# Kernel tuning notes

Hardware: AMD Instinct MI355X
Metric: run time of the kernel (lower is better)

The kernel has to match this reference:

```python
import jax, jax.numpy as jnp
import numpy as np

B, N, K, H, NI = 8, 4096, 32, 128, 384
SCALE = 30.0
EPS = 1e-5


def _ln(x, g, b):
    m = jnp.mean(x, axis=-1, keepdims=True)
    v = jnp.mean(jnp.square(x - m), axis=-1, keepdims=True)
    return (x - m) * jax.lax.rsqrt(v + EPS) * g + b


def setup_inputs() -> dict:
    key = jax.random.key(0)
    ks = jax.random.split(key, 20)
    w = lambda k, shape: jax.random.normal(k, shape, jnp.float32) * 0.02
    return {
        "h_V": jax.random.normal(ks[0], (B, N, H), jnp.float32),
        "h_E": jax.random.normal(ks[1], (B, N, K, NI), jnp.float32),
        "mask_V": (jax.random.uniform(ks[2], (B, N)) > 0.1).astype(jnp.float32),
        "mask_attend": (jax.random.uniform(ks[3], (B, N, K)) > 0.1).astype(jnp.float32),
        "W1_w": w(ks[4], (H, H + NI)), "W1_b": jnp.zeros((H,), jnp.float32),
        "W2_w": w(ks[5], (H, H)), "W2_b": jnp.zeros((H,), jnp.float32),
        "W3_w": w(ks[6], (H, H)), "W3_b": jnp.zeros((H,), jnp.float32),
        "ln1_g": jnp.ones((H,), jnp.float32), "ln1_b": jnp.zeros((H,), jnp.float32),
        "ln2_g": jnp.ones((H,), jnp.float32), "ln2_b": jnp.zeros((H,), jnp.float32),
        "Win_w": w(ks[7], (4 * H, H)), "Win_b": jnp.zeros((4 * H,), jnp.float32),
        "Wout_w": w(ks[8], (H, 4 * H)), "Wout_b": jnp.zeros((H,), jnp.float32),
    }


def reference(h_V, h_E, mask_V, mask_attend,
              W1_w, W1_b, W2_w, W2_b, W3_w, W3_b,
              ln1_g, ln1_b, ln2_g, ln2_b,
              Win_w, Win_b, Wout_w, Wout_b):
    gelu = lambda x: jax.nn.gelu(x, approximate=False)  # torch exact GELU
    # Split W1 across the broadcast (h_V) and per-edge (h_E) inputs instead of
    # materializing the [B,N,K,H+NI] concat: identical math, less memory.
    W1v, W1e = W1_w[:, :H], W1_w[:, H:]
    hv_part = jnp.einsum('bnh,oh->bno', h_V, W1v)              # [B,N,H]
    he_part = jnp.einsum('bnke,oe->bnko', h_E, W1e)            # [B,N,K,H]
    m = gelu(hv_part[:, :, None, :] + he_part + W1_b)
    m = gelu(jnp.einsum('bnkh,oh->bnko', m, W2_w) + W2_b)
    m = jnp.einsum('bnkh,oh->bnko', m, W3_w) + W3_b            # h_message
    m = mask_attend[..., None] * m
    dh = jnp.sum(m, axis=-2) / SCALE                           # [B,N,H]
    h = _ln(h_V + dh, ln1_g, ln1_b)
    ff = jnp.einsum('bnf,of->bno', gelu(jnp.einsum('bnh,fh->bnf', h, Win_w) + Win_b), Wout_w) + Wout_b
    h = _ln(h + ff, ln2_g, ln2_b)
    return mask_V[..., None] * h
```

## Files before the change

kernel.cpp:

```cpp
#include <hip/hip_runtime.h>

#define NODES 32768

typedef __attribute__((ext_vector_type(8))) short bf16x8;
typedef __attribute__((ext_vector_type(4))) float f32x4;

__device__ __forceinline__ unsigned short f2bf(float f) {
  __bf16 b = (__bf16)f;
  return __builtin_bit_cast(unsigned short, b);
}

__device__ __forceinline__ unsigned char f2fp8(float x) {
  int v = __builtin_amdgcn_cvt_pk_fp8_f32(x, x, 0, false);
  return (unsigned char)(v & 0xff);
}
__device__ __forceinline__ unsigned int pk4(f32x4 v) {
  int r = __builtin_amdgcn_cvt_pk_fp8_f32(v[0], v[1], 0, false);
  r = __builtin_amdgcn_cvt_pk_fp8_f32(v[2], v[3], r, true);
  return (unsigned int)r;
}

__device__ __forceinline__ float gelu_f(float x) {
  float e = __builtin_amdgcn_exp2f(-2.4558673f * x);
  return x * __builtin_amdgcn_rcpf(1.0f + e);
}

__device__ __forceinline__ f32x4 mfma16(bf16x8 a, bf16x8 b, f32x4 c) {
  return __builtin_amdgcn_mfma_f32_16x16x32_bf16(a, b, c, 0, 0, 0);
}
__device__ __forceinline__ f32x4 mfma8(long a, long b, f32x4 c) {
  return __builtin_amdgcn_mfma_f32_16x16x32_fp8_fp8(a, b, c, 0, 0, 0);
}

__global__ void DecLayer_54357106098674_kernel() {}

__global__ __launch_bounds__(256) void pack_kernel(
    const float* __restrict__ W, unsigned short* __restrict__ out,
    int ctiles, int ld, int koff) {
  int ct = blockIdx.x % ctiles;
  int ks = blockIdx.x / ctiles;
#pragma unroll
  for (int h = 0; h < 2; ++h) {
    int idx = threadIdx.x + h * 256;
    int j = idx & 7;
    int lane = idx >> 3;
    int o = ct * 16 + (lane & 15);
    int k = ks * 32 + ((lane >> 4) << 3) + j;
    out[((size_t)blockIdx.x * 64 + lane) * 8 + j] = f2bf(W[(size_t)o * ld + koff + k]);
  }
}

__global__ __launch_bounds__(256) void pack8_kernel(
    const float* __restrict__ W, unsigned char* __restrict__ out,
    int ctiles, int ld, int koff) {
  int ct = blockIdx.x % ctiles;
  int ks = blockIdx.x / ctiles;
#pragma unroll
  for (int h = 0; h < 2; ++h) {
    int idx = threadIdx.x + h * 256;
    int j = idx & 7;
    int lane = idx >> 3;
    int o = ct * 16 + (lane & 15);
    int k = ks * 32 + ((lane >> 4) << 3) + j;
    out[((size_t)blockIdx.x * 64 + lane) * 8 + j] = f2fp8(W[(size_t)o * ld + koff + k]);
  }
}

__global__ __launch_bounds__(256, 6) void edge_kernel(
    const float* __restrict__ hE, const float* __restrict__ hV,
    const float* __restrict__ maskA,
    const unsigned short* __restrict__ W1vp,
    const unsigned char* __restrict__ W1e8,
    const unsigned char* __restrict__ W2p8,
    const unsigned char* __restrict__ W3p8,
    const float* __restrict__ W1bias,
    const float* __restrict__ W2bias, const float* __restrict__ W3bias,
    const float* __restrict__ ln1g, const float* __restrict__ ln1b,
    float* __restrict__ hb) {
  __shared__ __align__(16) unsigned char A8[64 * 392];
  __shared__ __align__(16) unsigned short hvb[2][136];
  __shared__ float mkl[64];
  unsigned char* m1 = A8;
  unsigned char* m2 = A8 + 8704;
  float* red2 = (float*)(A8 + 17408);

  const int t = threadIdx.x;
  const int pair = ((blockIdx.x & 7) << 11) | (blockIdx.x >> 3);
  const int node0 = pair * 2;
  const float* vb0 = hV + (size_t)node0 * 128;
  const float* vb1 = vb0 + 128;

  {
    const int rr = t >> 3, cc = t & 7;
    const f32x4* src = (const f32x4*)(hE + (size_t)node0 * 12288) + rr * 96 + cc;
    unsigned char* dst0 = &A8[rr * 392 + cc * 4];
#pragma unroll
    for (int i = 0; i < 12; ++i) {
      f32x4 v = __builtin_nontemporal_load(src + i * 8);
      *(unsigned int*)(dst0 + i * 32) = pk4(v);
    }
    const f32x4* src1 = src + 32 * 96;
    unsigned char* dst1 = &A8[(rr + 32) * 392 + cc * 4];
#pragma unroll
    for (int i = 0; i < 12; ++i) {
      f32x4 v = __builtin_nontemporal_load(src1 + i * 8);
      *(unsigned int*)(dst1 + i * 32) = pk4(v);
    }
  }
  if (t < 64) {
    int nn = t >> 5, s = t & 31;
    f32x4 v = ((const f32x4*)(hV + (size_t)(node0 + nn) * 128))[s];
    ushort4 u;
    u.x = f2bf(v[0]); u.y = f2bf(v[1]); u.z = f2bf(v[2]); u.w = f2bf(v[3]);
    *(ushort4*)&hvb[nn][s * 4] = u;
  } else if (t < 128) {
    int q = t - 64;
    mkl[q] = maskA[(size_t)node0 * 32 + q];
  }
  __syncthreads();

  const int w = t >> 6, l = t & 63, lr = l & 15, lk = l >> 4;
  const int ct0 = w * 2, ct1 = w * 2 + 1;
  const int c0 = ct0 * 16 + lr, c1 = ct1 * 16 + lr;

  f32x4 g0[4], g1[4];
#pragma unroll
  for (int rt = 0; rt < 4; ++rt) {
    g0[rt] = (f32x4){0.f, 0.f, 0.f, 0.f};
    g1[rt] = (f32x4){0.f, 0.f, 0.f, 0.f};
  }
#pragma unroll
  for (int ks = 0; ks < 4; ++ks) {
    bf16x8 w0 = *(const bf16x8*)&W1vp[((size_t)(ks * 8 + ct0) * 64 + l) * 8];
    bf16x8 w1 = *(const bf16x8*)&W1vp[((size_t)(ks * 8 + ct1) * 64 + l) * 8];
#pragma unroll
    for (int rt = 0; rt < 4; ++rt) {
      bf16x8 a = *(const bf16x8*)&hvb[rt >> 1][ks * 32 + lk * 8];
      g0[rt] = mfma16(a, w0, g0[rt]);
      g1[rt] = mfma16(a, w1, g1[rt]);
    }
  }
#pragma unroll
  for (int ks = 0; ks < 12; ++ks) {
    long w0 = *(const long*)&W1e8[((size_t)(ks * 8 + ct0) * 64 + l) * 8];
    long w1 = *(const long*)&W1e8[((size_t)(ks * 8 + ct1) * 64 + l) * 8];
#pragma unroll
    for (int rt = 0; rt < 4; ++rt) {
      long a = *(const long*)&A8[(rt * 16 + lr) * 392 + ks * 32 + lk * 8];
      g0[rt] = mfma8(a, w0, g0[rt]);
      g1[rt] = mfma8(a, w1, g1[rt]);
    }
  }
  __syncthreads();

  {
    float bb0 = W1bias[c0], bb1 = W1bias[c1];
#pragma unroll
    for (int rt = 0; rt < 4; ++rt) {
#pragma unroll
      for (int r = 0; r < 4; ++r) {
        int row = rt * 16 + lk * 4 + r;
        m1[row * 136 + c0] = f2fp8(gelu_f(g0[rt][r] + bb0));
        m1[row * 136 + c1] = f2fp8(gelu_f(g1[rt][r] + bb1));
      }
    }
  }
  __syncthreads();

  f32x4 d0[4], d1[4];
#pragma unroll
  for (int rt = 0; rt < 4; ++rt) {
    d0[rt] = (f32x4){0.f, 0.f, 0.f, 0.f};
    d1[rt] = (f32x4){0.f, 0.f, 0.f, 0.f};
  }
#pragma unroll
  for (int ks = 0; ks < 4; ++ks) {
    long w0 = *(const long*)&W2p8[((size_t)(ks * 8 + ct0) * 64 + l) * 8];
    long w1 = *(const long*)&W2p8[((size_t)(ks * 8 + ct1) * 64 + l) * 8];
#pragma unroll
    for (int rt = 0; rt < 4; ++rt) {
      long a = *(const long*)&m1[(rt * 16 + lr) * 136 + ks * 32 + lk * 8];
      d0[rt] = mfma8(a, w0, d0[rt]);
      d1[rt] = mfma8(a, w1, d1[rt]);
    }
  }
  {
    float bb0 = W2bias[c0], bb1 = W2bias[c1];
#pragma unroll
    for (int rt = 0; rt < 4; ++rt) {
#pragma unroll
      for (int r = 0; r < 4; ++r) {
        int row = rt * 16 + lk * 4 + r;
        m2[row * 136 + c0] = f2fp8(gelu_f(d0[rt][r] + bb0));
        m2[row * 136 + c1] = f2fp8(gelu_f(d1[rt][r] + bb1));
      }
    }
  }
  __syncthreads();

  f32x4 e0[4], e1[4];
#pragma unroll
  for (int rt = 0; rt < 4; ++rt) {
    e0[rt] = (f32x4){0.f, 0.f, 0.f, 0.f};
    e1[rt] = (f32x4){0.f, 0.f, 0.f, 0.f};
  }
#pragma unroll
  for (int ks = 0; ks < 4; ++ks) {
    long w0 = *(const long*)&W3p8[((size_t)(ks * 8 + ct0) * 64 + l) * 8];
    long w1 = *(const long*)&W3p8[((size_t)(ks * 8 + ct1) * 64 + l) * 8];
#pragma unroll
    for (int rt = 0; rt < 4; ++rt) {
      long a = *(const long*)&m2[(rt * 16 + lr) * 136 + ks * 32 + lk * 8];
      e0[rt] = mfma8(a, w0, e0[rt]);
      e1[rt] = mfma8(a, w1, e1[rt]);
    }
  }

  {
    float b30 = W3bias[c0], b31 = W3bias[c1];
    float cs00 = 0.f, cs01 = 0.f, cs10 = 0.f, cs11 = 0.f;
#pragma unroll
    for (int r = 0; r < 4; ++r) {
      float mka = mkl[lk * 4 + r];
      float mkb = mkl[16 + lk * 4 + r];
      float mkc = mkl[32 + lk * 4 + r];
      float mkd = mkl[48 + lk * 4 + r];
      cs00 += mka * (e0[0][r] + b30) + mkb * (e0[1][r] + b30);
      cs01 += mka * (e1[0][r] + b31) + mkb * (e1[1][r] + b31);
      cs10 += mkc * (e0[2][r] + b30) + mkd * (e0[3][r] + b30);
      cs11 += mkc * (e1[2][r] + b31) + mkd * (e1[3][r] + b31);
    }
    cs00 += __shfl_xor(cs00, 16); cs00 += __shfl_xor(cs00, 32);
    cs01 += __shfl_xor(cs01, 16); cs01 += __shfl_xor(cs01, 32);
    cs10 += __shfl_xor(cs10, 16); cs10 += __shfl_xor(cs10, 32);
    cs11 += __shfl_xor(cs11, 16); cs11 += __shfl_xor(cs11, 32);
    if (lk == 0) {
      red2[c0]       = vb0[c0] + cs00 * (1.0f / 30.0f);
      red2[c1]       = vb0[c1] + cs01 * (1.0f / 30.0f);
      red2[128 + c0] = vb1[c0] + cs10 * (1.0f / 30.0f);
      red2[128 + c1] = vb1[c1] + cs11 * (1.0f / 30.0f);
    }
  }
  __syncthreads();

  {
    const int nn = w >> 1, ww = w & 1;
    const float* rn = red2 + nn * 128;
    float v0 = rn[l], v1 = rn[l + 64];
    float s = v0 + v1, sq = v0 * v0 + v1 * v1;
#pragma unroll
    for (int off = 1; off < 64; off <<= 1) {
      s += __shfl_xor(s, off);
      sq += __shfl_xor(sq, off);
    }
    float mean = s * (1.0f / 128.0f);
    float var = sq * (1.0f / 128.0f) - mean * mean;
    float rs = rsqrtf(var + 1e-5f);
    size_t ob = (size_t)(node0 + nn) * 128;
    if (ww == 0)
      hb[ob + l] = (v0 - mean) * rs * ln1g[l] + ln1b[l];
    else
      hb[ob + 64 + l] = (v1 - mean) * rs * ln1g[64 + l] + ln1b[64 + l];
  }
}

__global__ __launch_bounds__(256) void ffn_kernel(
    const float* h,
    const unsigned short* __restrict__ Winp,
    const unsigned short* __restrict__ Woutp,
    const float* __restrict__ Winbias, const float* __restrict__ Woutbias,
    const float* __restrict__ ln2g, const float* __restrict__ ln2b,
    const float* __restrict__ maskV, float* out) {
  __shared__ __align__(16) unsigned short hA[32 * 136];
  __shared__ __align__(16) unsigned short tl[32 * 520];
  __shared__ float mn[32], rstd[32], mv[32];
  float* ol = (float*)tl;

  const int t = threadIdx.x;
  const size_t base = (size_t)blockIdx.x * 32 * 128;

#pragma unroll
  for (int i = 0; i < 4; ++i) {
    int q = t + i * 256;
    int row = q >> 5, c4 = q & 31;
    f32x4 v = ((const f32x4*)(h + base))[q];
    ushort4 u;
    u.x = f2bf(v[0]); u.y = f2bf(v[1]); u.z = f2bf(v[2]); u.w = f2bf(v[3]);
    *(ushort4*)&hA[row * 136 + c4 * 4] = u;
  }
  if (t < 32) mv[t] = maskV[(size_t)blockIdx.x * 32 + t];
  __syncthreads();

  const int w = t >> 6, l = t & 63, lr = l & 15, lk = l >> 4;

  f32x4 p0[8], p1[8];
#pragma unroll
  for (int j = 0; j < 8; ++j) { p0[j] = (f32x4){0.f,0.f,0.f,0.f}; p1[j] = (f32x4){0.f,0.f,0.f,0.f}; }
#pragma unroll
  for (int ks = 0; ks < 4; ++ks) {
    bf16x8 a0 = *(const bf16x8*)&hA[lr * 136 + ks * 32 + lk * 8];
    bf16x8 a1 = *(const bf16x8*)&hA[(16 + lr) * 136 + ks * 32 + lk * 8];
#pragma unroll
    for (int j = 0; j < 8; ++j) {
      bf16x8 bv = *(const bf16x8*)&Winp[((size_t)(ks * 32 + (w * 8 + j)) * 64 + l) * 8];
      p0[j] = mfma16(a0, bv, p0[j]);
      p1[j] = mfma16(a1, bv, p1[j]);
    }
  }
#pragma unroll
  for (int j = 0; j < 8; ++j) {
    int col = (w * 8 + j) * 16 + lr;
    float bb = Winbias[col];
#pragma unroll
    for (int r = 0; r < 4; ++r) {
      tl[(lk * 4 + r) * 520 + col] = f2bf(gelu_f(p0[j][r] + bb));
      tl[(16 + lk * 4 + r) * 520 + col] = f2bf(gelu_f(p1[j][r] + bb));
    }
  }
  __syncthreads();

  const int ct0 = w * 2, ct1 = w * 2 + 1;
  const int c0 = ct0 * 16 + lr, c1 = ct1 * 16 + lr;
  f32x4 d00 = {0.f,0.f,0.f,0.f}, d01 = {0.f,0.f,0.f,0.f};
  f32x4 d10 = {0.f,0.f,0.f,0.f}, d11 = {0.f,0.f,0.f,0.f};
#pragma unroll
  for (int ks = 0; ks < 16; ++ks) {
    bf16x8 a0 = *(const bf16x8*)&tl[lr * 520 + ks * 32 + lk * 8];
    bf16x8 a1 = *(const bf16x8*)&tl[(16 + lr) * 520 + ks * 32 + lk * 8];
    bf16x8 w0 = *(const bf16x8*)&Woutp[((size_t)(ks * 8 + ct0) * 64 + l) * 8];
    bf16x8 w1 = *(const bf16x8*)&Woutp[((size_t)(ks * 8 + ct1) * 64 + l) * 8];
    d00 = mfma16(a0, w0, d00);
    d01 = mfma16(a0, w1, d01);
    d10 = mfma16(a1, w0, d10);
    d11 = mfma16(a1, w1, d11);
  }
  __syncthreads();
  {
    float bo0 = Woutbias[c0], bo1 = Woutbias[c1];
#pragma unroll
    for (int r = 0; r < 4; ++r) {
      int r0 = lk * 4 + r, r1 = 16 + lk * 4 + r;
      ol[r0 * 132 + c0] = d00[r] + bo0 + h[base + (size_t)r0 * 128 + c0];
      ol[r0 * 132 + c1] = d01[r] + bo1 + h[base + (size_t)r0 * 128 + c1];
      ol[r1 * 132 + c0] = d10[r] + bo0 + h[base + (size_t)r1 * 128 + c0];
      ol[r1 * 132 + c1] = d11[r] + bo1 + h[base + (size_t)r1 * 128 + c1];
    }
  }
  __syncthreads();

  {
    int row = t >> 3, p = t & 7;
    float s = 0.f, sq = 0.f;
#pragma unroll
    for (int i = 0; i < 16; ++i) {
      float x = ol[row * 132 + p * 16 + i];
      s += x; sq += x * x;
    }
    s += __shfl_xor(s, 1); sq += __shfl_xor(sq, 1);
    s += __shfl_xor(s, 2); sq += __shfl_xor(sq, 2);
    s += __shfl_xor(s, 4); sq += __shfl_xor(sq, 4);
    if (p == 0) {
      float mean = s * (1.0f / 128.0f);
      mn[row] = mean;
      rstd[row] = rsqrtf(sq * (1.0f / 128.0f) - mean * mean + 1e-5f);
    }
  }
  __syncthreads();

#pragma unroll
  for (int i = 0; i < 4; ++i) {
    int q = t + i * 256;
    int row = q >> 5, c = (q & 31) * 4;
    float m_ = mn[row], rs_ = rstd[row], mvv = mv[row];
    const float* orow = &ol[row * 132];
    f32x4 o;
    o[0] = mvv * ((orow[c + 0] - m_) * rs_ * ln2g[c + 0] + ln2b[c + 0]);
    o[1] = mvv * ((orow[c + 1] - m_) * rs_ * ln2g[c + 1] + ln2b[c + 1]);
    o[2] = mvv * ((orow[c + 2] - m_) * rs_ * ln2g[c + 2] + ln2b[c + 2]);
    o[3] = mvv * ((orow[c + 3] - m_) * rs_ * ln2g[c + 3] + ln2b[c + 3]);
    ((f32x4*)(out + base))[q] = o;
  }
}

extern "C" void kernel_launch(void* const* d_in, const int* in_sizes, int n_in,
                              void* d_out, int out_size, void* d_ws, size_t ws_size,
                              hipStream_t stream) {
  (void)in_sizes; (void)n_in; (void)out_size; (void)ws_size;
  const float* h_V   = (const float*)d_in[0];
  const float* h_E   = (const float*)d_in[1];
  const float* maskV = (const float*)d_in[2];
  const float* maskA = (const float*)d_in[3];
  const float* W1w   = (const float*)d_in[4];
  const float* W1b   = (const float*)d_in[5];
  const float* W2w   = (const float*)d_in[6];
  const float* W2b   = (const float*)d_in[7];
  const float* W3w   = (const float*)d_in[8];
  const float* W3b   = (const float*)d_in[9];
  const float* g1    = (const float*)d_in[10];
  const float* b1    = (const float*)d_in[11];
  const float* g2    = (const float*)d_in[12];
  const float* b2    = (const float*)d_in[13];
  const float* Winw  = (const float*)d_in[14];
  const float* Winb  = (const float*)d_in[15];
  const float* Woutw = (const float*)d_in[16];
  const float* Woutb = (const float*)d_in[17];
  float* out = (float*)d_out;

  char* ws = (char*)d_ws;
  unsigned short* W1vp  = (unsigned short*)(ws + 0);
  unsigned short* Winp  = (unsigned short*)(ws + 32768);
  unsigned short* Woutp = (unsigned short*)(ws + 163840);
  unsigned char*  W1e8  = (unsigned char*)(ws + 294912);
  unsigned char*  W2p8  = (unsigned char*)(ws + 344064);
  unsigned char*  W3p8  = (unsigned char*)(ws + 360448);

  pack_kernel <<<32,  256, 0, stream>>>(W1w,   W1vp,  8, 512, 0);
  pack8_kernel<<<96,  256, 0, stream>>>(W1w,   W1e8,  8, 512, 128);
  pack8_kernel<<<32,  256, 0, stream>>>(W2w,   W2p8,  8, 128, 0);
  pack8_kernel<<<32,  256, 0, stream>>>(W3w,   W3p8,  8, 128, 0);
  pack_kernel <<<128, 256, 0, stream>>>(Winw,  Winp, 32, 128, 0);
  pack_kernel <<<128, 256, 0, stream>>>(Woutw, Woutp, 8, 512, 0);

  edge_kernel<<<NODES / 2, 256, 0, stream>>>(h_E, h_V, maskA, W1vp, W1e8,
                                             W2p8, W3p8, W1b, W2b, W3b,
                                             g1, b1, out);
  ffn_kernel<<<NODES / 32, 256, 0, stream>>>(out, Winp, Woutp, Winb, Woutb,
                                             g2, b2, maskV, out);
}
```

Before: 373.8 us.

## Process edge nodes one at a time to halve LDS staging and raise occupancy

The edge kernel now stages only one node's 32 edges of fp8 h_E at a time in LDS, where before it held both nodes' 64 edges. The second node's load overlaps with the first node's GELU epilogue. Accumulator arrays shrink from 4 to 2 row tiles per stage, and launch bounds go from 6 to 7 blocks per CU, aiming at lower LDS and register use and higher occupancy. In exchange the W1 weight fragments are reloaded twice per block, and the extra phases add syncthreads.

Measured after the change: 507.4 us. 35.7% more time.

```diff
diff --git a/kernel.cpp b/kernel.cpp
--- a/kernel.cpp
+++ b/kernel.cpp
@@ -66,7 +66,7 @@
   }
 }
 
-__global__ __launch_bounds__(256, 6) void edge_kernel(
+__global__ __launch_bounds__(256, 7) void edge_kernel(
     const float* __restrict__ hE, const float* __restrict__ hV,
     const float* __restrict__ maskA,
     const unsigned short* __restrict__ W1vp,
@@ -77,12 +77,12 @@
     const float* __restrict__ W2bias, const float* __restrict__ W3bias,
     const float* __restrict__ ln1g, const float* __restrict__ ln1b,
     float* __restrict__ hb) {
-  __shared__ __align__(16) unsigned char A8[64 * 392];
+  __shared__ __align__(16) unsigned char A8[32 * 392];
+  __shared__ __align__(16) unsigned char m1s[64 * 136];
   __shared__ __align__(16) unsigned short hvb[2][136];
   __shared__ float mkl[64];
-  unsigned char* m1 = A8;
-  unsigned char* m2 = A8 + 8704;
-  float* red2 = (float*)(A8 + 17408);
+  unsigned char* m2 = A8;
+  float* red2 = (float*)(A8 + 8704);
 
   const int t = threadIdx.x;
   const int pair = ((blockIdx.x & 7) << 11) | (blockIdx.x >> 3);
@@ -90,22 +90,14 @@
   const float* vb0 = hV + (size_t)node0 * 128;
   const float* vb1 = vb0 + 128;
 
-  {
-    const int rr = t >> 3, cc = t & 7;
-    const f32x4* src = (const f32x4*)(hE + (size_t)node0 * 12288) + rr * 96 + cc;
-    unsigned char* dst0 = &A8[rr * 392 + cc * 4];
-#pragma unroll
-    for (int i = 0; i < 12; ++i) {
-      f32x4 v = __builtin_nontemporal_load(src + i * 8);
-      *(unsigned int*)(dst0 + i * 32) = pk4(v);
-    }
-    const f32x4* src1 = src + 32 * 96;
-    unsigned char* dst1 = &A8[(rr + 32) * 392 + cc * 4];
-#pragma unroll
-    for (int i = 0; i < 12; ++i) {
-      f32x4 v = __builtin_nontemporal_load(src1 + i * 8);
-      *(unsigned int*)(dst1 + i * 32) = pk4(v);
-    }
+  const int rr = t >> 3, cc = t & 7;
+  const f32x4* esrc0 = (const f32x4*)(hE + (size_t)node0 * 12288) + rr * 96 + cc;
+  unsigned char* adst = &A8[rr * 392 + cc * 4];
+
+#pragma unroll
+  for (int i = 0; i < 12; ++i) {
+    f32x4 v = __builtin_nontemporal_load(esrc0 + i * 8);
+    *(unsigned int*)(adst + i * 32) = pk4(v);
   }
   if (t < 64) {
     int nn = t >> 5, s = t & 31;
@@ -122,22 +114,23 @@
   const int w = t >> 6, l = t & 63, lr = l & 15, lk = l >> 4;
   const int ct0 = w * 2, ct1 = w * 2 + 1;
   const int c0 = ct0 * 16 + lr, c1 = ct1 * 16 + lr;
-
-  f32x4 g0[4], g1[4];
-#pragma unroll
-  for (int rt = 0; rt < 4; ++rt) {
-    g0[rt] = (f32x4){0.f, 0.f, 0.f, 0.f};
-    g1[rt] = (f32x4){0.f, 0.f, 0.f, 0.f};
+  const float bb10 = W1bias[c0], bb11 = W1bias[c1];
+
+  f32x4 g0[2], g1[2];
+#pragma unroll
+  for (int j = 0; j < 2; ++j) {
+    g0[j] = (f32x4){0.f, 0.f, 0.f, 0.f};
+    g1[j] = (f32x4){0.f, 0.f, 0.f, 0.f};
   }
 #pragma unroll
   for (int ks = 0; ks < 4; ++ks) {
+    bf16x8 a = *(const bf16x8*)&hvb[0][ks * 32 + lk * 8];
     bf16x8 w0 = *(const bf16x8*)&W1vp[((size_t)(ks * 8 + ct0) * 64 + l) * 8];
     bf16x8 w1 = *(const bf16x8*)&W1vp[((size_t)(ks * 8 + ct1) * 64 + l) * 8];
 #pragma unroll
-    for (int rt = 0; rt < 4; ++rt) {
-      bf16x8 a = *(const bf16x8*)&hvb[rt >> 1][ks * 32 + lk * 8];
-      g0[rt] = mfma16(a, w0, g0[rt]);
-      g1[rt] = mfma16(a, w1, g1[rt]);
+    for (int j = 0; j < 2; ++j) {
+      g0[j] = mfma16(a, w0, g0[j]);
+      g1[j] = mfma16(a, w1, g1[j]);
     }
   }
 #pragma unroll
@@ -145,100 +138,140 @@
     long w0 = *(const long*)&W1e8[((size_t)(ks * 8 + ct0) * 64 + l) * 8];
     long w1 = *(const long*)&W1e8[((size_t)(ks * 8 + ct1) * 64 + l) * 8];
 #pragma unroll
-    for (int rt = 0; rt < 4; ++rt) {
-      long a = *(const long*)&A8[(rt * 16 + lr) * 392 + ks * 32 + lk * 8];
-      g0[rt] = mfma8(a, w0, g0[rt]);
-      g1[rt] = mfma8(a, w1, g1[rt]);
-    }
-  }
-  __syncthreads();
-
-  {
-    float bb0 = W1bias[c0], bb1 = W1bias[c1];
-#pragma unroll
-    for (int rt = 0; rt < 4; ++rt) {
-#pragma unroll
-      for (int r = 0; r < 4; ++r) {
-        int row = rt * 16 + lk * 4 + r;
-        m1[row * 136 + c0] = f2fp8(gelu_f(g0[rt][r] + bb0));
-        m1[row * 136 + c1] = f2fp8(gelu_f(g1[rt][r] + bb1));
-      }
-    }
-  }
-  __syncthreads();
-
-  f32x4 d0[4], d1[4];
-#pragma unroll
-  for (int rt = 0; rt < 4; ++rt) {
-    d0[rt] = (f32x4){0.f, 0.f, 0.f, 0.f};
-    d1[rt] = (f32x4){0.f, 0.f, 0.f, 0.f};
+    for (int j = 0; j < 2; ++j) {
+      long a = *(const long*)&A8[(j * 16 + lr) * 392 + ks * 32 + lk * 8];
+      g0[j] = mfma8(a, w0, g0[j]);
+      g1[j] = mfma8(a, w1, g1[j]);
+    }
+  }
+  __syncthreads();
+
+#pragma unroll
+  for (int i = 0; i < 12; ++i) {
+    f32x4 v = __builtin_nontemporal_load(esrc0 + 32 * 96 + i * 8);
+    *(unsigned int*)(adst + i * 32) = pk4(v);
+  }
+#pragma unroll
+  for (int j = 0; j < 2; ++j) {
+#pragma unroll
+    for (int r = 0; r < 4; ++r) {
+      int row = j * 16 + lk * 4 + r;
+      m1s[row * 136 + c0] = f2fp8(gelu_f(g0[j][r] + bb10));
+      m1s[row * 136 + c1] = f2fp8(gelu_f(g1[j][r] + bb11));
+    }
+  }
+  __syncthreads();
+
+#pragma unroll
+  for (int j = 0; j < 2; ++j) {
+    g0[j] = (f32x4){0.f, 0.f, 0.f, 0.f};
+    g1[j] = (f32x4){0.f, 0.f, 0.f, 0.f};
   }
 #pragma unroll
   for (int ks = 0; ks < 4; ++ks) {
-    long w0 = *(const long*)&W2p8[((size_t)(ks * 8 + ct0) * 64 + l) * 8];
-    long w1 = *(const long*)&W2p8[((size_t)(ks * 8 + ct1) * 64 + l) * 8];
-#pragma unroll
-    for (int rt = 0; rt < 4; ++rt) {
-      long a = *(const long*)&m1[(rt * 16 + lr) * 136 + ks * 32 + lk * 8];
-      d0[rt] = mfma8(a, w0, d0[rt]);
-      d1[rt] = mfma8(a, w1, d1[rt]);
-    }
-  }
+    bf16x8 a = *(const bf16x8*)&hvb[1][ks * 32 + lk * 8];
+    bf16x8 w0 = *(const bf16x8*)&W1vp[((size_t)(ks * 8 + ct0) * 64 + l) * 8];
+    bf16x8 w1 = *(const bf16x8*)&W1vp[((size_t)(ks * 8 + ct1) * 64 + l) * 8];
+#pragma unroll
+    for (int j = 0; j < 2; ++j) {
+      g0[j] = mfma16(a, w0, g0[j]);
+      g1[j] = mfma16(a, w1, g1[j]);
+    }
+  }
+#pragma unroll
+  for (int ks = 0; ks < 12; ++ks) {
+    long w0 = *(const long*)&W1e8[((size_t)(ks * 8 + ct0) * 64 + l) * 8];
+    long w1 = *(const long*)&W1e8[((size_t)(ks * 8 + ct1) * 64 + l) * 8];
+#pragma unroll
+    for (int j = 0; j < 2; ++j) {
+      long a = *(const long*)&A8[(j * 16 + lr) * 392 + ks * 32 + lk * 8];
+      g0[j] = mfma8(a, w0, g0[j]);
+      g1[j] = mfma8(a, w1, g1[j]);
+    }
+  }
+  __syncthreads();
+
+#pragma unroll
+  for (int j = 0; j < 2; ++j) {
+#pragma unroll
+    for (int r = 0; r < 4; ++r) {
+      int row = 32 + j * 16 + lk * 4 + r;
+      m1s[row * 136 + c0] = f2fp8(gelu_f(g0[j][r] + bb10));
+      m1s[row * 136 + c1] = f2fp8(gelu_f(g1[j][r] + bb11));
+    }
+  }
+  __syncthreads();
+
   {
     float bb0 = W2bias[c0], bb1 = W2bias[c1];
 #pragma unroll
-    for (int rt = 0; rt < 4; ++rt) {
-#pragma unroll
-      for (int r = 0; r < 4; ++r) {
-        int row = rt * 16 + lk * 4 + r;
-        m2[row * 136 + c0] = f2fp8(gelu_f(d0[rt][r] + bb0));
-        m2[row * 136 + c1] = f2fp8(gelu_f(d1[rt][r] + bb1));
-      }
-    }
-  }
-  __syncthreads();
-
-  f32x4 e0[4], e1[4];
-#pragma unroll
-  for (int rt = 0; rt < 4; ++rt) {
-    e0[rt] = (f32x4){0.f, 0.f, 0.f, 0.f};
-    e1[rt] = (f32x4){0.f, 0.f, 0.f, 0.f};
-  }
-#pragma unroll
-  for (int ks = 0; ks < 4; ++ks) {
-    long w0 = *(const long*)&W3p8[((size_t)(ks * 8 + ct0) * 64 + l) * 8];
-    long w1 = *(const long*)&W3p8[((size_t)(ks * 8 + ct1) * 64 + l) * 8];
-#pragma unroll
-    for (int rt = 0; rt < 4; ++rt) {
-      long a = *(const long*)&m2[(rt * 16 + lr) * 136 + ks * 32 + lk * 8];
-      e0[rt] = mfma8(a, w0, e0[rt]);
-      e1[rt] = mfma8(a, w1, e1[rt]);
-    }
-  }
+    for (int p = 0; p < 2; ++p) {
+      f32x4 d0[2], d1[2];
+#pragma unroll
+      for (int j = 0; j < 2; ++j) {
+        d0[j] = (f32x4){0.f, 0.f, 0.f, 0.f};
+        d1[j] = (f32x4){0.f, 0.f, 0.f, 0.f};
+      }
+#pragma unroll
+      for (int ks = 0; ks < 4; ++ks) {
+        long w0 = *(const long*)&W2p8[((size_t)(ks * 8 + ct0) * 64 + l) * 8];
+        long w1 = *(const long*)&W2p8[((size_t)(ks * 8 + ct1) * 64 + l) * 8];
+#pragma unroll
+        for (int j = 0; j < 2; ++j) {
+          long a = *(const long*)&m1s[(p * 32 + j * 16 + lr) * 136 + ks * 32 + lk * 8];
+          d0[j] = mfma8(a, w0, d0[j]);
+          d1[j] = mfma8(a, w1, d1[j]);
+        }
+      }
+#pragma unroll
+      for (int j = 0; j < 2; ++j) {
+#pragma unroll
+        for (int r = 0; r < 4; ++r) {
+          int row = p * 32 + j * 16 + lk * 4 + r;
+          m2[row * 136 + c0] = f2fp8(gelu_f(d0[j][r] + bb0));
+          m2[row * 136 + c1] = f2fp8(gelu_f(d1[j][r] + bb1));
+        }
+      }
+    }
+  }
+  __syncthreads();
 
   {
     float b30 = W3bias[c0], b31 = W3bias[c1];
-    float cs00 = 0.f, cs01 = 0.f, cs10 = 0.f, cs11 = 0.f;
-#pragma unroll
-    for (int r = 0; r < 4; ++r) {
-      float mka = mkl[lk * 4 + r];
-      float mkb = mkl[16 + lk * 4 + r];
-      float mkc = mkl[32 + lk * 4 + r];
-      float mkd = mkl[48 + lk * 4 + r];
-      cs00 += mka * (e0[0][r] + b30) + mkb * (e0[1][r] + b30);
-      cs01 += mka * (e1[0][r] + b31) + mkb * (e1[1][r] + b31);
-      cs10 += mkc * (e0[2][r] + b30) + mkd * (e0[3][r] + b30);
-      cs11 += mkc * (e1[2][r] + b31) + mkd * (e1[3][r] + b31);
-    }
-    cs00 += __shfl_xor(cs00, 16); cs00 += __shfl_xor(cs00, 32);
-    cs01 += __shfl_xor(cs01, 16); cs01 += __shfl_xor(cs01, 32);
-    cs10 += __shfl_xor(cs10, 16); cs10 += __shfl_xor(cs10, 32);
-    cs11 += __shfl_xor(cs11, 16); cs11 += __shfl_xor(cs11, 32);
-    if (lk == 0) {
-      red2[c0]       = vb0[c0] + cs00 * (1.0f / 30.0f);
-      red2[c1]       = vb0[c1] + cs01 * (1.0f / 30.0f);
-      red2[128 + c0] = vb1[c0] + cs10 * (1.0f / 30.0f);
-      red2[128 + c1] = vb1[c1] + cs11 * (1.0f / 30.0f);
+#pragma unroll
+    for (int p = 0; p < 2; ++p) {
+      f32x4 e0[2], e1[2];
+#pragma unroll
+      for (int j = 0; j < 2; ++j) {
+        e0[j] = (f32x4){0.f, 0.f, 0.f, 0.f};
+        e1[j] = (f32x4){0.f, 0.f, 0.f, 0.f};
+      }
+#pragma unroll
+      for (int ks = 0; ks < 4; ++ks) {
+        long w0 = *(const long*)&W3p8[((size_t)(ks * 8 + ct0) * 64 + l) * 8];
+        long w1 = *(const long*)&W3p8[((size_t)(ks * 8 + ct1) * 64 + l) * 8];
+#pragma unroll
+        for (int j = 0; j < 2; ++j) {
+          long a = *(const long*)&m2[(p * 32 + j * 16 + lr) * 136 + ks * 32 + lk * 8];
+          e0[j] = mfma8(a, w0, e0[j]);
+          e1[j] = mfma8(a, w1, e1[j]);
+        }
+      }
+      float cs0 = 0.f, cs1 = 0.f;
+#pragma unroll
+      for (int r = 0; r < 4; ++r) {
+        float mka = mkl[p * 32 + lk * 4 + r];
+        float mkb = mkl[p * 32 + 16 + lk * 4 + r];
+        cs0 += mka * (e0[0][r] + b30) + mkb * (e0[1][r] + b30);
+        cs1 += mka * (e1[0][r] + b31) + mkb * (e1[1][r] + b31);
+      }
+      cs0 += __shfl_xor(cs0, 16); cs0 += __shfl_xor(cs0, 32);
+      cs1 += __shfl_xor(cs1, 16); cs1 += __shfl_xor(cs1, 32);
+      if (lk == 0) {
+        const float* vbn = (p == 0) ? vb0 : vb1;
+        red2[p * 128 + c0] = vbn[c0] + cs0 * (1.0f / 30.0f);
+        red2[p * 128 + c1] = vbn[c1] + cs1 * (1.0f / 30.0f);
+      }
     }
   }
   __syncthreads();
```
